# Optimization experiments

Measured on AMD Instinct MI355X. Metric: run time of the kernel, lower is better.

Reference implementation:

```python
import jax, jax.numpy as jnp
import numpy as np

WS, OWS, HEADS, DH = 8, 12, 4, 16
INNER = HEADS * DH
DIM = 64
RATIO = 0.5
REL = 12  # rel_size = WS + (OWS - WS)


def _conv1x1(x, W, b):
    return jnp.einsum('oc,bchw->bohw', W, x) + b[None, :, None, None]


def _lrelu(x):
    return jnp.where(x >= 0, x, 0.1 * x)


def _rel_to_abs(x):
    # x: [b, l, 2r-1] -> [b, l, r]
    b, l, m = x.shape
    r = (m + 1) // 2
    x = jnp.pad(x, ((0, 0), (0, 0), (0, 1))).reshape(b, l * (m + 1))
    x = jnp.pad(x, ((0, 0), (0, m - l))).reshape(b, l + 1, m)
    return x[:, :l, -r:]


def _relative_logits_1d(q, rel_k):
    # q: [b, h, w, d], rel_k: [2r-1, d] -> [b, h, r, w, r]
    b, h, w, _ = q.shape
    r = (rel_k.shape[0] + 1) // 2
    logits = jnp.einsum('bxyd,rd->bxyr', q, rel_k)
    logits = _rel_to_abs(logits.reshape(b * h, w, 2 * r - 1)).reshape(b, h, w, r)
    return jnp.broadcast_to(logits[:, :, None], (b, h, r, w, r))


def _rel_pos_emb(q, rel_h, rel_w):
    # q: [b, WS*WS, DH] -> [b, WS*WS, REL*REL]
    b = q.shape[0]
    q = q.reshape(b, WS, WS, DH)
    lw = _relative_logits_1d(q, rel_w)                        # [b, x, i, y, j]
    lw = lw.transpose(0, 1, 3, 2, 4).reshape(b, WS * WS, REL * REL)   # (x y),(i j)
    lh = _relative_logits_1d(q.transpose(0, 2, 1, 3), rel_h)  # [b, y, i, x, j]
    lh = lh.transpose(0, 3, 1, 4, 2).reshape(b, WS * WS, REL * REL)   # (x y),(j i)
    return lw + lh


def _windows(t, B, Hw, Ww):
    # 'b c (h p1) (w p2) -> b (h w) (p1 p2 c)'
    return t.reshape(B, INNER, Hw, WS, Ww, WS).transpose(0, 2, 4, 3, 5, 1).reshape(B, Hw * Ww, WS * WS * INNER)


def _forward(x, condition_global, Wq, bq, Wk, bk, Wv, bv, Wout, bout,
             rel_h, rel_w, pin_W, pin_b, ln_w, ln_b, sa_W, sa_b,
             m1_W, m1_b, m2_W, m2_b):
    B, C, H, W = x.shape
    Hw, Ww = H // WS, W // WS
    Nw = Hw * Ww
    keep = int(Nw * RATIO)  # deterministic num_keep_node (expected r=0.5)
    scale = DH ** -0.5

    qs = _conv1x1(x, Wq, bq)
    ks = _conv1x1(x, Wk, bk)
    vs = _conv1x1(x, Wv, bv)

    # condition_wind: stacked ij meshgrid of linspace(-1,1,WS), tiled over windows
    lin = jnp.linspace(-1.0, 1.0, WS)
    gy, gx = jnp.meshgrid(lin, lin, indexing='ij')
    wind = jnp.tile(jnp.stack([gy, gx]).astype(x.dtype)[None], (B, 1, Hw, Ww))
    cond = jnp.concatenate([vs, condition_global, wind], axis=1)  # [B, INNER+4, H, W]

    # PredictorLG
    h1 = _conv1x1(cond, pin_W, pin_b)
    u = h1.mean(1, keepdims=True)
    s = ((h1 - u) ** 2).mean(1, keepdims=True)
    h1 = ln_w[None, :, None, None] * (h1 - u) / jnp.sqrt(s + 1e-6) + ln_b[None, :, None, None]
    h1 = _lrelu(h1)
    sa = jax.lax.conv_general_dilated(h1, sa_W, (1, 1), ((1, 1), (1, 1)),
                                      dimension_numbers=('NCHW', 'OIHW', 'NCHW'))
    sa = jax.nn.sigmoid(sa + sa_b[None, :, None, None])          # [B,1,H,W]

    xm = h1.mean(1)                                               # [B,H,W]
    xm = xm.reshape(B, Hw, WS, Ww, WS).transpose(0, 1, 3, 2, 4).reshape(B, Nw, WS * WS)
    z = _lrelu(xm @ m1_W.T + m1_b)
    pred = jax.nn.softmax(z @ m2_W.T + m2_b, axis=-1)
    score = pred[:, :, 0]
    idx = jnp.argsort(-score, axis=1)
    idx1, idx2 = idx[:, :keep], idx[:, keep:]
    bar = jnp.arange(B)[:, None]

    v_easy = vs * sa

    qw = _windows(qs, B, Hw, Ww)                                  # [B, Nw, 64*INNER]

    pad = (OWS - WS) // 2
    def unfold(t):
        p = jax.lax.conv_general_dilated_patches(t, (OWS, OWS), (WS, WS),
                                                 [(pad, pad), (pad, pad)])
        # [B, INNER*OWS*OWS, Hw, Ww], channel-major (c, kh, kw) like torch unfold
        p = p.reshape(B, INNER, OWS * OWS, Nw)
        return p.transpose(0, 3, 2, 1).reshape(B, Nw, OWS * OWS * INNER)  # (j c)
    kw, vw = unfold(ks), unfold(vs)

    qk, kk, vk = qw[bar, idx1], kw[bar, idx1], vw[bar, idx1]       # gather hard windows

    def heads(t, ntok):
        return t.reshape(B * keep, ntok, HEADS, DH).transpose(0, 2, 1, 3).reshape(B * keep * HEADS, ntok, DH)
    qh = heads(qk, WS * WS) * scale
    kh = heads(kk, OWS * OWS)
    vh = heads(vk, OWS * OWS)

    attn = jnp.einsum('bqc,bkc->bqk', qh, kh) + _rel_pos_emb(qh, rel_h, rel_w)
    attn = jax.nn.softmax(attn, axis=-1)
    vo = jnp.einsum('bqk,bkc->bqc', attn, vh)                      # [B*keep*HEADS, 64, DH]

    # '(b j head) (p1 p2) c -> b j (p1 p2 head c)'
    v1 = vo.reshape(B, keep, HEADS, WS * WS, DH).transpose(0, 1, 3, 2, 4).reshape(B, keep, WS * WS * INNER)
    v2 = _windows(v_easy, B, Hw, Ww)[bar, idx2]

    out = jnp.zeros((B, Nw, WS * WS * INNER), x.dtype)
    out = out.at[bar, idx1].set(v1).at[bar, idx2].set(v2)          # batch_index_fill
    # 'b (h w) (dh dw c) -> b c (h dh) (w dw)'
    out = out.reshape(B, Hw, Ww, WS, WS, INNER).transpose(0, 5, 1, 3, 2, 4).reshape(B, INNER, H, W)
    return _conv1x1(out, Wout, bout)


def setup_inputs() -> dict:
    key = jax.random.key(0)
    k = jax.random.split(key, 16)
    B, H, W = 2, 256, 256
    cdim = INNER + 4
    rel_scale = DH ** -0.5

    def p(kk, shape, s=0.05):
        return jax.random.normal(kk, shape, jnp.float32) * s

    return {
        'x': jax.random.normal(k[0], (B, DIM, H, W), jnp.float32),
        'condition_global': jax.random.normal(k[1], (B, 2, H, W), jnp.float32),
        'Wq': p(k[2], (INNER, DIM)), 'bq': jnp.zeros((INNER,), jnp.float32),
        'Wk': p(k[3], (INNER, DIM)), 'bk': jnp.zeros((INNER,), jnp.float32),
        'Wv': p(k[4], (INNER, DIM)), 'bv': jnp.zeros((INNER,), jnp.float32),
        'Wout': p(k[5], (DIM, INNER)), 'bout': jnp.zeros((DIM,), jnp.float32),
        'rel_h': jax.random.normal(k[6], (2 * REL - 1, DH), jnp.float32) * rel_scale,
        'rel_w': jax.random.normal(k[7], (2 * REL - 1, DH), jnp.float32) * rel_scale,
        'pin_W': p(k[8], (cdim // 4, cdim)), 'pin_b': jnp.zeros((cdim // 4,), jnp.float32),
        'ln_w': jnp.ones((cdim // 4,), jnp.float32), 'ln_b': jnp.zeros((cdim // 4,), jnp.float32),
        'sa_W': p(k[9], (1, cdim // 4, 3, 3)), 'sa_b': jnp.zeros((1,), jnp.float32),
        'm1_W': p(k[10], (WS, WS * WS)), 'm1_b': jnp.zeros((WS,), jnp.float32),
        'm2_W': p(k[11], (2, WS)), 'm2_b': jnp.zeros((2,), jnp.float32),
    }


def reference(x, condition_global, Wq, bq, Wk, bk, Wv, bv, Wout, bout,
              rel_h, rel_w, pin_W, pin_b, ln_w, ln_b, sa_W, sa_b,
              m1_W, m1_b, m2_W, m2_b):
    return _forward(x, condition_global, Wq, bq, Wk, bk, Wv, bv, Wout, bout,
                    rel_h, rel_w, pin_W, pin_b, ln_w, ln_b, sa_W, sa_b,
                    m1_W, m1_b, m2_W, m2_b)
```

## Files before the change

kernel.cpp:

```cpp
#include <hip/hip_runtime.h>
#include <math.h>

#define NPIX   65536
#define NPIXT  131072
#define NW     1024
#define KEEP   512


__device__ __forceinline__ float bcast(float v, int l) {
    return __int_as_float(__builtin_amdgcn_readlane(__float_as_int(v), l));
}

__global__ __launch_bounds__(256) void k_qkv(
    const float* __restrict__ x,
    const float* __restrict__ Wq, const float* __restrict__ bq,
    const float* __restrict__ Wk, const float* __restrict__ bk,
    const float* __restrict__ Wv, const float* __restrict__ bv,
    float* __restrict__ qs, float* __restrict__ ks, float* __restrict__ vs)
{
    const int tid  = threadIdx.x;
    const int lane = tid & 63;
    const int og   = __builtin_amdgcn_readfirstlane(tid >> 6);
    const int tile = blockIdx.x;
    const int b    = tile >> 9;
    const int p0   = (tile & 511) << 7;
    const int p    = p0 + 2 * lane;
    const int gp   = (b << 16) + p;
    const int wo   = og * 16;

    const float* Ws[3]   = {Wq, Wk, Wv};
    const float* bias[3] = {bq, bk, bv};
    float* outs[3] = {qs + (size_t)gp * 64, ks + (size_t)gp * 64, vs + (size_t)gp * 64};
    const float* xg = x + ((size_t)b * 64) * NPIX + p;

    #pragma unroll
    for (int m = 0; m < 3; ++m) {
        const float* Wm = Ws[m];
        float w[16];
        #pragma unroll
        for (int j = 0; j < 16; ++j) w[j] = Wm[(wo + j) * 64 + lane];

        float acc0[16], acc1[16];
        #pragma unroll
        for (int j = 0; j < 16; ++j) { acc0[j] = 0.f; acc1[j] = 0.f; }

        #pragma unroll 8
        for (int c = 0; c < 64; ++c) {
            const float2 xv = *(const float2*)(xg + (size_t)c * NPIX);
            #pragma unroll
            for (int j = 0; j < 16; ++j) {
                const float wv = bcast(w[j], c);
                acc0[j] += wv * xv.x;
                acc1[j] += wv * xv.y;
            }
        }

        const float* bb = bias[m];
        float* o0 = outs[m];
        #pragma unroll
        for (int j4 = 0; j4 < 4; ++j4) {
            float4 v0, v1;
            v0.x = acc0[j4*4+0] + bb[wo + j4*4+0]; v1.x = acc1[j4*4+0] + bb[wo + j4*4+0];
            v0.y = acc0[j4*4+1] + bb[wo + j4*4+1]; v1.y = acc1[j4*4+1] + bb[wo + j4*4+1];
            v0.z = acc0[j4*4+2] + bb[wo + j4*4+2]; v1.z = acc1[j4*4+2] + bb[wo + j4*4+2];
            v0.w = acc0[j4*4+3] + bb[wo + j4*4+3]; v1.w = acc1[j4*4+3] + bb[wo + j4*4+3];
            *(float4*)(o0 + wo + j4*4)      = v0;
            *(float4*)(o0 + 64 + wo + j4*4) = v1;
        }
    }
}

__global__ __launch_bounds__(256) void k_cond(
    const float* __restrict__ vs, const float* __restrict__ cg,
    const float* __restrict__ pinW, const float* __restrict__ pinb,
    const float* __restrict__ lnw, const float* __restrict__ lnb,
    float* __restrict__ h1, float* __restrict__ xm)
{
    const int gp = blockIdx.x * 256 + threadIdx.x;
    const int b  = gp >> 16;
    const int p  = gp & 65535;
    const int h  = p >> 8;
    const int w  = p & 255;

    float acc[17];
    #pragma unroll
    for (int oc = 0; oc < 17; ++oc) acc[oc] = pinb[oc];

    const float* vp = vs + (size_t)gp * 64;
    #pragma unroll 8
    for (int c4 = 0; c4 < 16; ++c4) {
        const float4 v4 = *(const float4*)(vp + c4 * 4);
        const float vv[4] = {v4.x, v4.y, v4.z, v4.w};
        #pragma unroll
        for (int k = 0; k < 4; ++k) {
            const int c = c4 * 4 + k;
            #pragma unroll
            for (int oc = 0; oc < 17; ++oc)
                acc[oc] += pinW[oc * 68 + c] * vv[k];
        }
    }
    const float c64 = cg[(b * 2 + 0) * NPIX + p];
    const float c65 = cg[(b * 2 + 1) * NPIX + p];
    const float c66 = -1.f + 2.f * (float)(h & 7) / 7.f;
    const float c67 = -1.f + 2.f * (float)(w & 7) / 7.f;
    #pragma unroll
    for (int oc = 0; oc < 17; ++oc)
        acc[oc] += pinW[oc * 68 + 64] * c64 + pinW[oc * 68 + 65] * c65 +
                   pinW[oc * 68 + 66] * c66 + pinW[oc * 68 + 67] * c67;

    float u = 0.f;
    #pragma unroll
    for (int oc = 0; oc < 17; ++oc) u += acc[oc];
    u *= (1.f / 17.f);
    float s = 0.f;
    #pragma unroll
    for (int oc = 0; oc < 17; ++oc) { const float d = acc[oc] - u; s += d * d; }
    s *= (1.f / 17.f);
    const float rstd = rsqrtf(s + 1e-6f);

    float xsum = 0.f;
    #pragma unroll
    for (int oc = 0; oc < 17; ++oc) {
        float hv = lnw[oc] * (acc[oc] - u) * rstd + lnb[oc];
        hv = (hv >= 0.f) ? hv : 0.1f * hv;
        h1[(b * 17 + oc) * NPIX + p] = hv;
        xsum += hv;
    }
    const int win = (h >> 3) * 32 + (w >> 3);
    const int idx = ((h & 7) << 3) | (w & 7);
    xm[(b << 16) + win * 64 + idx] = xsum * (1.f / 17.f);
}

__global__ __launch_bounds__(256) void k_sa(
    const float* __restrict__ h1, const float* __restrict__ saW,
    const float* __restrict__ sab, float* __restrict__ sa)
{
    __shared__ float S[17 * 3 * 256];
    const int tid = threadIdx.x;
    const int b   = blockIdx.x >> 8;
    const int row = blockIdx.x & 255;

    for (int i = tid; i < 3264; i += 256) {
        const int ch  = i / 192;
        const int rem = i - ch * 192;
        const int dr  = rem >> 6;
        const int c4  = rem & 63;
        const int rr  = row + dr - 1;
        float4 v = {0.f, 0.f, 0.f, 0.f};
        if ((unsigned)rr < 256u)
            v = *(const float4*)(h1 + ((size_t)(b * 17 + ch)) * NPIX + rr * 256 + c4 * 4);
        *(float4*)&S[(ch * 3 + dr) * 256 + c4 * 4] = v;
    }
    __syncthreads();

    const int w = tid;
    float acc = sab[0];
    #pragma unroll 1
    for (int ch = 0; ch < 17; ++ch) {
        #pragma unroll
        for (int dr = 0; dr < 3; ++dr) {
            const float* Sp = &S[(ch * 3 + dr) * 256];
            const float m  = Sp[w];
            const float l  = (w > 0)   ? Sp[w - 1] : 0.f;
            const float r_ = (w < 255) ? Sp[w + 1] : 0.f;
            const float* Wp = saW + (ch * 3 + dr) * 3;
            acc += Wp[0] * l + Wp[1] * m + Wp[2] * r_;
        }
    }
    sa[b * NPIX + row * 256 + w] = 1.f / (1.f + __expf(-acc));
}

__global__ __launch_bounds__(1024) void k_score_select(
    const float* __restrict__ xm,
    const float* __restrict__ m1W, const float* __restrict__ m1b,
    const float* __restrict__ m2W, const float* __restrict__ m2b,
    int* __restrict__ flag, int* __restrict__ kept)
{
    __shared__ float sc[NW];
    const int b = blockIdx.x;
    const int t = threadIdx.x;

    float z[8];
    #pragma unroll
    for (int jj = 0; jj < 8; ++jj) z[jj] = m1b[jj];

    const float* xw = xm + (b << 16) + t * 64;
    #pragma unroll 4
    for (int t4 = 0; t4 < 16; ++t4) {
        const float4 v4 = *(const float4*)(xw + t4 * 4);
        const float vv[4] = {v4.x, v4.y, v4.z, v4.w};
        #pragma unroll
        for (int k = 0; k < 4; ++k) {
            const int tt = t4 * 4 + k;
            #pragma unroll
            for (int jj = 0; jj < 8; ++jj)
                z[jj] += m1W[jj * 64 + tt] * vv[k];
        }
    }
    #pragma unroll
    for (int jj = 0; jj < 8; ++jj) z[jj] = (z[jj] >= 0.f) ? z[jj] : 0.1f * z[jj];

    float l0 = m2b[0], l1 = m2b[1];
    #pragma unroll
    for (int jj = 0; jj < 8; ++jj) { l0 += m2W[jj] * z[jj]; l1 += m2W[8 + jj] * z[jj]; }
    const float mx = fmaxf(l0, l1);
    const float e0 = expf(l0 - mx), e1 = expf(l1 - mx);
    sc[t] = e0 / (e0 + e1);
    __syncthreads();

    const float s = sc[t];
    int cnt = 0;
    for (int jq = 0; jq < NW; jq += 4) {
        const float4 s4 = *(const float4*)&sc[jq];
        cnt += (s4.x > s) || (s4.x == s && (jq + 0) < t);
        cnt += (s4.y > s) || (s4.y == s && (jq + 1) < t);
        cnt += (s4.z > s) || (s4.z == s && (jq + 2) < t);
        cnt += (s4.w > s) || (s4.w == s && (jq + 3) < t);
    }
    flag[b * NW + t] = (cnt < KEEP) ? 1 : 0;
    if (cnt < KEEP) kept[b * KEEP + cnt] = t;
}

__global__ __launch_bounds__(64) void k_attn(
    const float* __restrict__ qs, const float* __restrict__ ks,
    const float* __restrict__ vs, const int* __restrict__ kept,
    const float* __restrict__ relh, const float* __restrict__ relw,
    float* __restrict__ amix)
{
    const int b    = blockIdx.z;
    const int head = blockIdx.y;
    const int win  = kept[b * KEEP + blockIdx.x];
    const int wy = win >> 5, wx = win & 31;
    const int lane = threadIdx.x;
    const int choff = head * 16;
    const size_t bbase = (size_t)b * NPIX;
    const int px0 = (wy * 8) * 256 + wx * 8;
    const int qrow = lane >> 3, qcol = lane & 7;
    const int sub = lane >> 4, d_ = lane & 15;

    float q[16];
    {
        const float* qp = qs + (bbase + px0 + qrow * 256 + qcol) * 64 + choff;
        #pragma unroll
        for (int j4 = 0; j4 < 4; ++j4) {
            const float4 v = *(const float4*)(qp + j4 * 4);
            q[j4 * 4 + 0] = v.x * 0.25f; q[j4 * 4 + 1] = v.y * 0.25f;
            q[j4 * 4 + 2] = v.z * 0.25f; q[j4 * 4 + 3] = v.w * 0.25f;
        }
    }

    float cw[12];
    #pragma unroll
    for (int k = 0; k < 12; ++k) {
        const float* rw = relw + (k - qcol + 11) * 16;
        float sw = 0.f;
        #pragma unroll
        for (int j4 = 0; j4 < 4; ++j4) {
            const float4 w4 = *(const float4*)(rw + j4 * 4);
            sw += q[j4*4+0]*w4.x + q[j4*4+1]*w4.y + q[j4*4+2]*w4.z + q[j4*4+3]*w4.w;
        }
        cw[k] = sw;
    }

    const int wy8 = wy * 8 - 2, wx8 = wx * 8 - 2;
    const int laneoff = choff + d_;

    float sum = 0.f;
    float vo[16];
    #pragma unroll
    for (int d = 0; d < 16; ++d) vo[d] = 0.f;

    #pragma unroll 1
    for (int r = 0; r < 12; ++r) {
        const int ry = wy8 + r;
        const bool rowok = (unsigned)ry < 256u;

        const float* rh = relh + (r - qrow + 11) * 16;
        float srow = 0.f;
        #pragma unroll
        for (int j4 = 0; j4 < 4; ++j4) {
            const float4 h4 = *(const float4*)(rh + j4 * 4);
            srow += q[j4*4+0]*h4.x + q[j4*4+1]*h4.y + q[j4*4+2]*h4.z + q[j4*4+3]*h4.w;
        }

        #pragma unroll
        for (int gi = 0; gi < 3; ++gi) {
            const int cx = wx8 + 4 * gi + sub;
            float kg = 0.f, vg = 0.f;
            if (rowok && (unsigned)cx < 256u) {
                const size_t a = (bbase + (size_t)(ry * 256 + cx)) * 64 + laneoff;
                kg = ks[a];
                vg = vs[a];
            }
            #pragma unroll
            for (int kk = 0; kk < 4; ++kk) {
                float s = srow + cw[4 * gi + kk];
                #pragma unroll
                for (int d = 0; d < 16; ++d)
                    s += bcast(kg, kk * 16 + d) * q[d];
                const float e = __expf(s);
                sum += e;
                #pragma unroll
                for (int d = 0; d < 16; ++d)
                    vo[d] += e * bcast(vg, kk * 16 + d);
            }
        }
    }

    const float inv = 1.f / sum;
    float* op = amix + (bbase + px0 + qrow * 256 + qcol) * 64 + choff;
    #pragma unroll
    for (int j4 = 0; j4 < 4; ++j4) {
        float4 v;
        v.x = vo[j4*4+0] * inv; v.y = vo[j4*4+1] * inv;
        v.z = vo[j4*4+2] * inv; v.w = vo[j4*4+3] * inv;
        *(float4*)(op + j4 * 4) = v;
    }
}

__global__ __launch_bounds__(256) void k_out_f(
    const float* __restrict__ amix, const float* __restrict__ vs,
    const float* __restrict__ sa, const int* __restrict__ flag,
    const float* __restrict__ W, const float* __restrict__ bias,
    float* __restrict__ out)
{
    __shared__ float xs[64][130];
    __shared__ float smult[128];
    __shared__ int   sflag[128];
    const int tid  = threadIdx.x;
    const int lane = tid & 63;
    const int og   = __builtin_amdgcn_readfirstlane(tid >> 6);
    const int tile = blockIdx.x;
    const int b    = tile >> 9;
    const int p0   = (tile & 511) << 7;
    const int wo   = og * 16;

    if (tid < 128) {
        const int p   = p0 + tid;
        const int h   = p >> 8, w_ = p & 255;
        const int win = (h >> 3) * 32 + (w_ >> 3);
        const int fl  = flag[b * NW + win];
        sflag[tid] = fl;
        smult[tid] = fl ? 1.f : sa[(b << 16) + p];
    }
    __syncthreads();

    #pragma unroll
    for (int it = 0; it < 8; ++it) {
        const int i   = it * 256 + tid;
        const int pxl = i >> 4;
        const int c4  = i & 15;
        const int gpl = (b << 16) + p0 + pxl;
        const float* src = (sflag[pxl] ? amix : vs) + (size_t)gpl * 64;
        const float m = smult[pxl];
        const float4 v = *(const float4*)(src + c4 * 4);
        xs[c4 * 4 + 0][pxl] = v.x * m;
        xs[c4 * 4 + 1][pxl] = v.y * m;
        xs[c4 * 4 + 2][pxl] = v.z * m;
        xs[c4 * 4 + 3][pxl] = v.w * m;
    }
    __syncthreads();

    float w[16];
    #pragma unroll
    for (int j = 0; j < 16; ++j) w[j] = W[(wo + j) * 64 + lane];

    float acc0[16], acc1[16];
    #pragma unroll
    for (int j = 0; j < 16; ++j) { acc0[j] = 0.f; acc1[j] = 0.f; }

    #pragma unroll 8
    for (int c = 0; c < 64; ++c) {
        const float2 xv = *(const float2*)&xs[c][2 * lane];
        #pragma unroll
        for (int j = 0; j < 16; ++j) {
            const float wv = bcast(w[j], c);
            acc0[j] += wv * xv.x;
            acc1[j] += wv * xv.y;
        }
    }

    const int p    = p0 + 2 * lane;
    const int base = (b << 6) * NPIX + p;
    #pragma unroll
    for (int j = 0; j < 16; ++j) {
        const float bj = bias[wo + j];
        out[base +     (wo + j) * NPIX] = acc0[j] + bj;
        out[base + 1 + (wo + j) * NPIX] = acc1[j] + bj;
    }
}

extern "C" void kernel_launch(void* const* d_in, const int* in_sizes, int n_in,
                              void* d_out, int out_size, void* d_ws, size_t ws_size,
                              hipStream_t stream)
{
    const float* x    = (const float*)d_in[0];
    const float* cg   = (const float*)d_in[1];
    const float* Wq   = (const float*)d_in[2];
    const float* bq   = (const float*)d_in[3];
    const float* Wk   = (const float*)d_in[4];
    const float* bk   = (const float*)d_in[5];
    const float* Wv   = (const float*)d_in[6];
    const float* bv   = (const float*)d_in[7];
    const float* Wout = (const float*)d_in[8];
    const float* bout = (const float*)d_in[9];
    const float* relh = (const float*)d_in[10];
    const float* relw = (const float*)d_in[11];
    const float* pinW = (const float*)d_in[12];
    const float* pinb = (const float*)d_in[13];
    const float* lnw  = (const float*)d_in[14];
    const float* lnb  = (const float*)d_in[15];
    const float* saW  = (const float*)d_in[16];
    const float* sab  = (const float*)d_in[17];
    const float* m1W  = (const float*)d_in[18];
    const float* m1b  = (const float*)d_in[19];
    const float* m2W  = (const float*)d_in[20];
    const float* m2b  = (const float*)d_in[21];
    float* out = (float*)d_out;

    float* ws    = (float*)d_ws;
    float* qs    = ws;
    float* ks    = qs + 8388608;
    float* vs    = ks + 8388608;
    float* h1    = vs + 8388608;
    float* xm    = h1 + 17 * NPIXT;
    float* sa    = xm + NPIXT;
    int*   flag  = (int*)(sa + NPIXT);
    int*   kept  = flag + 2048;

    k_qkv         <<<1024, 256, 0, stream>>>(x, Wq, bq, Wk, bk, Wv, bv, qs, ks, vs);
    k_cond        <<<NPIXT / 256, 256, 0, stream>>>(vs, cg, pinW, pinb, lnw, lnb, h1, xm);
    k_sa          <<<512, 256, 0, stream>>>(h1, saW, sab, sa);
    k_score_select<<<2, 1024, 0, stream>>>(xm, m1W, m1b, m2W, m2b, flag, kept);
    k_attn        <<<dim3(KEEP, 4, 2), 64, 0, stream>>>(qs, ks, vs, kept, relh, relw, qs);
    k_out_f       <<<1024, 256, 0, stream>>>(qs, vs, sa, flag, Wout, bout, out);
}
```

Measured before the change: 441.3 us.

## Stage window keys in LDS for attention and broadcast pinW via readlane

The attention kernel now runs all four heads of a window in a single 256-thread block. It stages the 12x12 neighbourhood of keys into shared memory once and reads the key vectors from LDS with vector loads, replacing the per-element cross-lane broadcasts. The cond kernel preloads the projection weights into registers across the wavefront and fetches each weight with readlane instead of repeated scalar/global reads. The trade-off is a block-wide barrier and 36KB of LDS per block, which may limit occupancy.

After: 604.5 us. +37.0%, slower.

```diff
diff --git a/kernel.cpp b/kernel.cpp
--- a/kernel.cpp
+++ b/kernel.cpp
@@ -76,18 +76,27 @@
     const float* __restrict__ lnw, const float* __restrict__ lnb,
     float* __restrict__ h1, float* __restrict__ xm)
 {
-    const int gp = blockIdx.x * 256 + threadIdx.x;
+    const int tid  = threadIdx.x;
+    const int lane = tid & 63;
+    const int gp = blockIdx.x * 256 + tid;
     const int b  = gp >> 16;
     const int p  = gp & 65535;
     const int h  = p >> 8;
     const int w  = p & 255;
 
+    float pw[19];
+    #pragma unroll
+    for (int k = 0; k < 19; ++k) {
+        const int idx = k * 64 + lane;
+        pw[k] = (idx < 1156) ? pinW[idx] : 0.f;
+    }
+
     float acc[17];
     #pragma unroll
     for (int oc = 0; oc < 17; ++oc) acc[oc] = pinb[oc];
 
     const float* vp = vs + (size_t)gp * 64;
-    #pragma unroll 8
+    #pragma unroll 4
     for (int c4 = 0; c4 < 16; ++c4) {
         const float4 v4 = *(const float4*)(vp + c4 * 4);
         const float vv[4] = {v4.x, v4.y, v4.z, v4.w};
@@ -95,8 +104,10 @@
         for (int k = 0; k < 4; ++k) {
             const int c = c4 * 4 + k;
             #pragma unroll
-            for (int oc = 0; oc < 17; ++oc)
-                acc[oc] += pinW[oc * 68 + c] * vv[k];
+            for (int oc = 0; oc < 17; ++oc) {
+                const int idx = oc * 68 + c;
+                acc[oc] += bcast(pw[idx >> 6], idx & 63) * vv[k];
+            }
         }
     }
     const float c64 = cg[(b * 2 + 0) * NPIX + p];
@@ -104,9 +115,14 @@
     const float c66 = -1.f + 2.f * (float)(h & 7) / 7.f;
     const float c67 = -1.f + 2.f * (float)(w & 7) / 7.f;
     #pragma unroll
-    for (int oc = 0; oc < 17; ++oc)
-        acc[oc] += pinW[oc * 68 + 64] * c64 + pinW[oc * 68 + 65] * c65 +
-                   pinW[oc * 68 + 66] * c66 + pinW[oc * 68 + 67] * c67;
+    for (int oc = 0; oc < 17; ++oc) {
+        const int i64 = oc * 68 + 64, i65 = oc * 68 + 65;
+        const int i66 = oc * 68 + 66, i67 = oc * 68 + 67;
+        acc[oc] += bcast(pw[i64 >> 6], i64 & 63) * c64 +
+                   bcast(pw[i65 >> 6], i65 & 63) * c65 +
+                   bcast(pw[i66 >> 6], i66 & 63) * c66 +
+                   bcast(pw[i67 >> 6], i67 & 63) * c67;
+    }
 
     float u = 0.f;
     #pragma unroll
@@ -221,22 +237,40 @@
     if (cnt < KEEP) kept[b * KEEP + cnt] = t;
 }
 
-__global__ __launch_bounds__(64) void k_attn(
+__global__ __launch_bounds__(256, 4) void k_attn(
     const float* __restrict__ qs, const float* __restrict__ ks,
     const float* __restrict__ vs, const int* __restrict__ kept,
     const float* __restrict__ relh, const float* __restrict__ relw,
     float* __restrict__ amix)
 {
-    const int b    = blockIdx.z;
-    const int head = blockIdx.y;
+    __shared__ float SK[144 * 64];
+    const int b    = blockIdx.y;
     const int win  = kept[b * KEEP + blockIdx.x];
     const int wy = win >> 5, wx = win & 31;
-    const int lane = threadIdx.x;
+    const int tid  = threadIdx.x;
+    const int head = __builtin_amdgcn_readfirstlane(tid >> 6);
+    const int lane = tid & 63;
     const int choff = head * 16;
     const size_t bbase = (size_t)b * NPIX;
     const int px0 = (wy * 8) * 256 + wx * 8;
     const int qrow = lane >> 3, qcol = lane & 7;
     const int sub = lane >> 4, d_ = lane & 15;
+    const int wy8 = wy * 8 - 2, wx8 = wx * 8 - 2;
+
+    #pragma unroll
+    for (int it = 0; it < 9; ++it) {
+        const int i   = it * 256 + tid;
+        const int pxl = i >> 4;
+        const int c4  = i & 15;
+        const int rl  = pxl / 12;
+        const int col = pxl - rl * 12;
+        const int ry  = wy8 + rl;
+        const int cx  = wx8 + col;
+        float4 kv = {0.f, 0.f, 0.f, 0.f};
+        if ((unsigned)ry < 256u && (unsigned)cx < 256u)
+            kv = *(const float4*)(ks + (bbase + (size_t)(ry * 256 + cx)) * 64 + c4 * 4);
+        *(float4*)&SK[pxl * 64 + c4 * 4] = kv;
+    }
 
     float q[16];
     {
@@ -262,13 +296,14 @@
         cw[k] = sw;
     }
 
-    const int wy8 = wy * 8 - 2, wx8 = wx * 8 - 2;
     const int laneoff = choff + d_;
 
     float sum = 0.f;
     float vo[16];
     #pragma unroll
     for (int d = 0; d < 16; ++d) vo[d] = 0.f;
+
+    __syncthreads();
 
     #pragma unroll 1
     for (int r = 0; r < 12; ++r) {
@@ -286,23 +321,33 @@
         #pragma unroll
         for (int gi = 0; gi < 3; ++gi) {
             const int cx = wx8 + 4 * gi + sub;
-            float kg = 0.f, vg = 0.f;
-            if (rowok && (unsigned)cx < 256u) {
-                const size_t a = (bbase + (size_t)(ry * 256 + cx)) * 64 + laneoff;
-                kg = ks[a];
-                vg = vs[a];
-            }
+            float vg = 0.f;
+            if (rowok && (unsigned)cx < 256u)
+                vg = vs[(bbase + (size_t)(ry * 256 + cx)) * 64 + laneoff];
+
             #pragma unroll
             for (int kk = 0; kk < 4; ++kk) {
+                const float* kb = &SK[(r * 12 + 4 * gi + kk) * 64 + choff];
+                const float4 k0 = *(const float4*)(kb + 0);
+                const float4 k1 = *(const float4*)(kb + 4);
+                const float4 k2 = *(const float4*)(kb + 8);
+                const float4 k3 = *(const float4*)(kb + 12);
                 float s = srow + cw[4 * gi + kk];
-                #pragma unroll
-                for (int d = 0; d < 16; ++d)
-                    s += bcast(kg, kk * 16 + d) * q[d];
+                s += k0.x*q[0];  s += k0.y*q[1];  s += k0.z*q[2];  s += k0.w*q[3];
+                s += k1.x*q[4];  s += k1.y*q[5];  s += k1.z*q[6];  s += k1.w*q[7];
+                s += k2.x*q[8];  s += k2.y*q[9];  s += k2.z*q[10]; s += k2.w*q[11];
+                s += k3.x*q[12]; s += k3.y*q[13]; s += k3.z*q[14]; s += k3.w*q[15];
                 const float e = __expf(s);
                 sum += e;
+                float vd[8];
                 #pragma unroll
-                for (int d = 0; d < 16; ++d)
-                    vo[d] += e * bcast(vg, kk * 16 + d);
+                for (int d = 0; d < 8; ++d) vd[d] = bcast(vg, kk * 16 + d);
+                #pragma unroll
+                for (int d = 0; d < 8; ++d) vo[d] += e * vd[d];
+                #pragma unroll
+                for (int d = 0; d < 8; ++d) vd[d] = bcast(vg, kk * 16 + 8 + d);
+                #pragma unroll
+                for (int d = 0; d < 8; ++d) vo[8 + d] += e * vd[d];
             }
         }
     }
@@ -432,6 +477,6 @@
     k_cond        <<<NPIXT / 256, 256, 0, stream>>>(vs, cg, pinW, pinb, lnw, lnb, h1, xm);
     k_sa          <<<512, 256, 0, stream>>>(h1, saW, sab, sa);
     k_score_select<<<2, 1024, 0, stream>>>(xm, m1W, m1b, m2W, m2b, flag, kept);
-    k_attn        <<<dim3(KEEP, 4, 2), 64, 0, stream>>>(qs, ks, vs, kept, relh, relw, qs);
+    k_attn        <<<dim3(KEEP, 2), 256, 0, stream>>>(qs, ks, vs, kept, relh, relw, qs);
     k_out_f       <<<1024, 256, 0, stream>>>(qs, vs, sa, flag, Wout, bout, out);
 }
```
